# Performance work log

Hardware: AMD Instinct MI355X
Metric: run time of the kernel (lower is better)

Reference implementation:

```python
import jax, jax.numpy as jnp
import numpy as np

B, T, C, H = 4, 2048, 1024, 16
HD = C // H
INIT_SCALE = 0.25

def setup_inputs() -> dict:
    key = jax.random.key(0)
    k1, k2, k3 = jax.random.split(key, 3)
    x = jax.random.normal(k1, (B, T, C), dtype=jnp.float32)
    W_attn = jax.random.normal(k2, (3 * C, C), dtype=jnp.float32) * INIT_SCALE  # torch Linear weight [out,in]
    b_attn = jnp.zeros((3 * C,), dtype=jnp.float32)
    W_proj = jax.random.normal(k3, (C, C), dtype=jnp.float32) * INIT_SCALE
    b_proj = jnp.zeros((C,), dtype=jnp.float32)
    return {"x": x, "W_attn": W_attn, "b_attn": b_attn, "W_proj": W_proj, "b_proj": b_proj}

def reference(x, W_attn, b_attn, W_proj, b_proj):
    # fused QKV projection: [B,T,3C]
    qkv = x @ W_attn.T + b_attn
    q, k, v = jnp.split(qkv, 3, axis=-1)  # each [B,T,C]
    # [B,H,T,HD]
    q = q.reshape(B, T, H, HD).transpose(0, 2, 1, 3)
    k = k.reshape(B, T, H, HD).transpose(0, 2, 1, 3)
    v = v.reshape(B, T, H, HD).transpose(0, 2, 1, 3)
    scale = 1.0 / jnp.sqrt(jnp.asarray(HD, dtype=q.dtype))
    attn = jnp.einsum('bhqd,bhkd->bhqk', q, k) * scale  # [B,H,T,T]
    attn = jax.nn.softmax(attn, axis=-1)
    out = jnp.einsum('bhqk,bhkd->bhqd', attn, v)  # [B,H,T,HD]
    out = out.transpose(0, 2, 1, 3).reshape(B, T, C)
    return out @ W_proj.T + b_proj
```

## Files before the change

kernel.cpp:

```cpp
#include <hip/hip_runtime.h>
#include <hip/hip_bf16.h>

#define BB 4
#define TT 2048
#define CC 1024
#define HH 16
#define HD 64

typedef _Float16 half8 __attribute__((ext_vector_type(8)));
typedef _Float16 half4 __attribute__((ext_vector_type(4)));
typedef _Float16 half2_t __attribute__((ext_vector_type(2)));
typedef float floatx4 __attribute__((ext_vector_type(4)));

__device__ __forceinline__ void async_cp16(const void* g, void* l) {
    __builtin_amdgcn_global_load_lds(
        (const __attribute__((address_space(1))) unsigned int*)g,
        (__attribute__((address_space(3))) unsigned int*)l,
        16, 0, 0);
}

__global__ void cvt_f32_f16(const float* __restrict__ src, _Float16* __restrict__ dst, int n) {
    int i = (blockIdx.x * blockDim.x + threadIdx.x) * 8;
    if (i < n) {
        float4 v0 = *(const float4*)(src + i);
        float4 v1 = *(const float4*)(src + i + 4);
        half8 h;
        h[0] = (_Float16)v0.x; h[1] = (_Float16)v0.y; h[2] = (_Float16)v0.z; h[3] = (_Float16)v0.w;
        h[4] = (_Float16)v1.x; h[5] = (_Float16)v1.y; h[6] = (_Float16)v1.z; h[7] = (_Float16)v1.w;
        *(half8*)(dst + i) = h;
    }
}

template <int EPI>
__global__ __launch_bounds__(256) void hgemm_nt(
    const _Float16* __restrict__ A, const _Float16* __restrict__ Bw,
    const float* __restrict__ bias,
    _Float16* __restrict__ q_out, _Float16* __restrict__ k_out, _Float16* __restrict__ v_out,
    float* __restrict__ c_out,
    int M, int N, int K)
{
    __shared__ __attribute__((aligned(16))) _Float16 As[128 * 32];
    __shared__ __attribute__((aligned(16))) _Float16 Bs[128 * 32];

    const int tid  = threadIdx.x;
    const int lane = tid & 63;
    const int wave = tid >> 6;
    const int quad = lane >> 4;
    const int lc   = lane & 15;
    const int wr   = wave >> 1, wc = wave & 1;
    const size_t bm = (size_t)blockIdx.y * 128;
    const size_t bn = (size_t)blockIdx.x * 128;

    const int r0 = tid >> 2;
    const int ck = (tid & 3) * 8;

    const _Float16* Ap0 = A + (bm + r0) * (size_t)K + ck;
    const _Float16* Ap1 = A + (bm + 64 + r0) * (size_t)K + ck;
    const _Float16* Bp0 = Bw + (bn + r0) * (size_t)K + ck;
    const _Float16* Bp1 = Bw + (bn + 64 + r0) * (size_t)K + ck;
    _Float16* lA0 = As + tid * 8;
    _Float16* lA1 = As + 2048 + tid * 8;
    _Float16* lB0 = Bs + tid * 8;
    _Float16* lB1 = Bs + 2048 + tid * 8;

    floatx4 acc[4][4] = {};

    for (int kk = 0; kk < K; kk += 32) {
        __syncthreads();
        async_cp16(Ap0 + kk, lA0);
        async_cp16(Ap1 + kk, lA1);
        async_cp16(Bp0 + kk, lB0);
        async_cp16(Bp1 + kk, lB1);
        __syncthreads();

        half8 af[4], bf[4];
#pragma unroll
        for (int mt = 0; mt < 4; mt++) af[mt] = *(const half8*)(As + (wr * 64 + mt * 16 + lc) * 32 + quad * 8);
#pragma unroll
        for (int nt = 0; nt < 4; nt++) bf[nt] = *(const half8*)(Bs + (wc * 64 + nt * 16 + lc) * 32 + quad * 8);
#pragma unroll
        for (int mt = 0; mt < 4; mt++)
#pragma unroll
            for (int nt = 0; nt < 4; nt++)
                acc[mt][nt] = __builtin_amdgcn_mfma_f32_16x16x32_f16(af[mt], bf[nt], acc[mt][nt], 0, 0, 0);
    }

#pragma unroll
    for (int mt = 0; mt < 4; mt++) {
        int mbase = (int)bm + wr * 64 + mt * 16 + quad * 4;
#pragma unroll
        for (int nt = 0; nt < 4; nt++) {
            int n = (int)bn + wc * 64 + nt * 16 + lc;
            float bv = bias[n];
#pragma unroll
            for (int r = 0; r < 4; r++) {
                float v = acc[mt][nt][r] + bv;
                int mm = mbase + r;
                if (EPI == 0) {
                    int seg = n >> 10;
                    int cm  = n & 1023;
                    int h = cm >> 6, d = cm & 63;
                    int bb = mm >> 11, t = mm & 2047;
                    size_t dst = (((size_t)(bb * HH + h)) * TT + t) * HD + d;
                    if (seg == 0)      q_out[dst] = (_Float16)(v * 0.18033688f);
                    else if (seg == 1) k_out[dst] = (_Float16)v;
                    else               v_out[dst] = (_Float16)v;
                } else {
                    c_out[(size_t)mm * N + n] = v;
                }
            }
        }
    }
}

__global__ __launch_bounds__(512) void attn_flash(
    const _Float16* __restrict__ Qp, const _Float16* __restrict__ Kp,
    const _Float16* __restrict__ Vp, _Float16* __restrict__ Op)
{
    __shared__ __attribute__((aligned(16))) _Float16 Ks[64][72];
    __shared__ __attribute__((aligned(16))) _Float16 Vt[64][76];

    const int bh   = blockIdx.x;
    const int qt   = blockIdx.y;
    const int tid  = threadIdx.x;
    const int lane = tid & 63;
    const int wave = tid >> 6;
    const int quad = lane >> 4;
    const int lc   = lane & 15;

    const size_t hb = (size_t)bh * TT * HD;
    const _Float16* Kh = Kp + hb;
    const _Float16* Vh = Vp + hb;

    const int q0row = qt * 256 + wave * 32 + lc;
    const int q1row = q0row + 16;
    half8 bq00 = *(const half8*)(Qp + hb + (size_t)q0row * HD + quad * 8);
    half8 bq01 = *(const half8*)(Qp + hb + (size_t)q0row * HD + 32 + quad * 8);
    half8 bq10 = *(const half8*)(Qp + hb + (size_t)q1row * HD + quad * 8);
    half8 bq11 = *(const half8*)(Qp + hb + (size_t)q1row * HD + 32 + quad * 8);

    floatx4 o0[4] = {}, o1[4] = {};
    float m0 = -1e30f, l0 = 0.f, m1 = -1e30f, l1 = 0.f;

    const int sk  = tid >> 3;
    const int sc0 = (tid & 7) * 8;
    const int vkp = tid >> 4;
    const int vd4 = (tid & 15) * 4;

    const _Float16* Kg  = Kh + (size_t)sk * HD + sc0;
    const _Float16* Vg0 = Vh + (size_t)(2 * vkp) * HD + vd4;
    const _Float16* Vg1 = Vg0 + HD;

    for (int kt = 0; kt < TT; kt += 64) {
        const size_t koff = (size_t)kt * HD;
        half8 kv  = *(const half8*)(Kg + koff);
        half4 va0 = *(const half4*)(Vg0 + koff);
        half4 vb0 = *(const half4*)(Vg1 + koff);
        __syncthreads();
        *(half8*)&Ks[sk][sc0] = kv;
#pragma unroll
        for (int j = 0; j < 4; j++) {
            half2_t w; w[0] = va0[j]; w[1] = vb0[j];
            *(half2_t*)&Vt[vd4 + j][2 * vkp] = w;
        }
        __syncthreads();

        floatx4 s0[4], s1[4];
        const floatx4 zf = {0.f, 0.f, 0.f, 0.f};
#pragma unroll
        for (int m = 0; m < 4; m++) {
            half8 a0 = *(const half8*)&Ks[m * 16 + lc][quad * 8];
            half8 a1 = *(const half8*)&Ks[m * 16 + lc][32 + quad * 8];
            s0[m] = __builtin_amdgcn_mfma_f32_16x16x32_f16(a0, bq00, zf, 0, 0, 0);
            s0[m] = __builtin_amdgcn_mfma_f32_16x16x32_f16(a1, bq01, s0[m], 0, 0, 0);
            s1[m] = __builtin_amdgcn_mfma_f32_16x16x32_f16(a0, bq10, zf, 0, 0, 0);
            s1[m] = __builtin_amdgcn_mfma_f32_16x16x32_f16(a1, bq11, s1[m], 0, 0, 0);
        }

        half4 pf0[4], pf1[4];
        {
            float mx = s0[0][0];
#pragma unroll
            for (int m = 0; m < 4; m++)
#pragma unroll
                for (int r = 0; r < 4; r++) mx = fmaxf(mx, s0[m][r]);
            mx = fmaxf(mx, __shfl_xor(mx, 16));
            mx = fmaxf(mx, __shfl_xor(mx, 32));
            float mnew = fmaxf(m0, mx);
            float al = exp2f(m0 - mnew);
            m0 = mnew;
            float rs = 0.f;
#pragma unroll
            for (int m = 0; m < 4; m++) {
                float p0 = exp2f(s0[m][0] - mnew);
                float p1 = exp2f(s0[m][1] - mnew);
                float p2 = exp2f(s0[m][2] - mnew);
                float p3 = exp2f(s0[m][3] - mnew);
                rs += (p0 + p1) + (p2 + p3);
                half4 t;
                t[0] = (_Float16)p0; t[1] = (_Float16)p1;
                t[2] = (_Float16)p2; t[3] = (_Float16)p3;
                pf0[m] = t;
            }
            rs += __shfl_xor(rs, 16);
            rs += __shfl_xor(rs, 32);
            l0 = l0 * al + rs;
#pragma unroll
            for (int dt = 0; dt < 4; dt++) o0[dt] *= al;
        }
        {
            float mx = s1[0][0];
#pragma unroll
            for (int m = 0; m < 4; m++)
#pragma unroll
                for (int r = 0; r < 4; r++) mx = fmaxf(mx, s1[m][r]);
            mx = fmaxf(mx, __shfl_xor(mx, 16));
            mx = fmaxf(mx, __shfl_xor(mx, 32));
            float mnew = fmaxf(m1, mx);
            float al = exp2f(m1 - mnew);
            m1 = mnew;
            float rs = 0.f;
#pragma unroll
            for (int m = 0; m < 4; m++) {
                float p0 = exp2f(s1[m][0] - mnew);
                float p1 = exp2f(s1[m][1] - mnew);
                float p2 = exp2f(s1[m][2] - mnew);
                float p3 = exp2f(s1[m][3] - mnew);
                rs += (p0 + p1) + (p2 + p3);
                half4 t;
                t[0] = (_Float16)p0; t[1] = (_Float16)p1;
                t[2] = (_Float16)p2; t[3] = (_Float16)p3;
                pf1[m] = t;
            }
            rs += __shfl_xor(rs, 16);
            rs += __shfl_xor(rs, 32);
            l1 = l1 * al + rs;
#pragma unroll
            for (int dt = 0; dt < 4; dt++) o1[dt] *= al;
        }

#pragma unroll
        for (int dt = 0; dt < 4; dt++) {
            const _Float16* vr = &Vt[dt * 16 + lc][quad * 4];
#pragma unroll
            for (int m = 0; m < 4; m++) {
                half4 va = *(const half4*)(vr + m * 16);
                o0[dt] = __builtin_amdgcn_mfma_f32_16x16x16f16(va, pf0[m], o0[dt], 0, 0, 0);
                o1[dt] = __builtin_amdgcn_mfma_f32_16x16x16f16(va, pf1[m], o1[dt], 0, 0, 0);
            }
        }
    }

    const int b = bh >> 4, h = bh & 15;
    {
        float inv = 1.0f / l0;
        size_t base = ((size_t)(b * TT + q0row)) * CC + h * HD;
#pragma unroll
        for (int dt = 0; dt < 4; dt++) {
            half4 hv;
#pragma unroll
            for (int r = 0; r < 4; r++) hv[r] = (_Float16)(o0[dt][r] * inv);
            *(half4*)(Op + base + dt * 16 + quad * 4) = hv;
        }
    }
    {
        float inv = 1.0f / l1;
        size_t base = ((size_t)(b * TT + q1row)) * CC + h * HD;
#pragma unroll
        for (int dt = 0; dt < 4; dt++) {
            half4 hv;
#pragma unroll
            for (int r = 0; r < 4; r++) hv[r] = (_Float16)(o1[dt][r] * inv);
            *(half4*)(Op + base + dt * 16 + quad * 4) = hv;
        }
    }
}

extern "C" void kernel_launch(void* const* d_in, const int* in_sizes, int n_in,
                              void* d_out, int out_size, void* d_ws, size_t ws_size,
                              hipStream_t stream) {
    const float* x      = (const float*)d_in[0];
    const float* W_attn = (const float*)d_in[1];
    const float* b_attn = (const float*)d_in[2];
    const float* W_proj = (const float*)d_in[3];
    const float* b_proj = (const float*)d_in[4];
    float* out = (float*)d_out;

    const size_t SZ_XH  = (size_t)BB * TT * CC * 2;
    const size_t SZ_WA  = (size_t)3 * CC * CC * 2;
    const size_t SZ_WP  = (size_t)CC * CC * 2;
    const size_t SZ_QKV = (size_t)BB * HH * TT * HD * 2;
    size_t off = 0;
    _Float16* xh  = (_Float16*)((char*)d_ws + off); off += SZ_XH;
    _Float16* wah = (_Float16*)((char*)d_ws + off); off += SZ_WA;
    _Float16* wph = (_Float16*)((char*)d_ws + off); off += SZ_WP;
    _Float16* Qh  = (_Float16*)((char*)d_ws + off); off += SZ_QKV;
    _Float16* Kh  = (_Float16*)((char*)d_ws + off); off += SZ_QKV;
    _Float16* Vh  = (_Float16*)((char*)d_ws + off); off += SZ_QKV;
    _Float16* Ah  = (_Float16*)((char*)d_ws + off); off += SZ_XH;
    if (ws_size < off) return;

    const int NX  = BB * TT * CC;
    const int NWA = 3 * CC * CC;
    const int NWP = CC * CC;
    cvt_f32_f16<<<NX / 8 / 256, 256, 0, stream>>>(x, xh, NX);
    cvt_f32_f16<<<NWA / 8 / 256, 256, 0, stream>>>(W_attn, wah, NWA);
    cvt_f32_f16<<<NWP / 8 / 256, 256, 0, stream>>>(W_proj, wph, NWP);

    hgemm_nt<0><<<dim3(3 * CC / 128, BB * TT / 128), 256, 0, stream>>>(
        xh, wah, b_attn, Qh, Kh, Vh, nullptr, BB * TT, 3 * CC, CC);

    attn_flash<<<dim3(BB * HH, TT / 256), 512, 0, stream>>>(Qh, Kh, Vh, Ah);

    hgemm_nt<1><<<dim3(CC / 128, BB * TT / 128), 256, 0, stream>>>(
        Ah, wph, b_proj, nullptr, nullptr, nullptr, out, BB * TT, CC, CC);
}
```

Before: 326.5 us.

## Double-buffer GEMM LDS tiles and prefetch next K/V tile in attention

The GEMM kernel now uses two LDS buffers. It issues the async global-to-LDS copy for the next 32-wide K chunk before computing on the current one, so loads overlap the MFMA work instead of stalling between barriers. The attention kernel register-prefetches the next K/V tile right after the LDS store barrier, hiding global latency behind the QK/softmax/PV compute. This costs double the GEMM LDS footprint and extra live registers in attention, which may reduce occupancy. The GEMM relies on the async copy completing by the next __syncthreads, with no explicit vmcnt wait.

```diff
diff --git a/kernel.cpp b/kernel.cpp
--- a/kernel.cpp
+++ b/kernel.cpp
@@ -31,6 +31,28 @@
     }
 }
 
+#define GEMM_CP(base, koffs)                                      \
+    async_cp16(Ap0 + (koffs), (base) + tid * 8);                  \
+    async_cp16(Ap1 + (koffs), (base) + 2048 + tid * 8);           \
+    async_cp16(Bp0 + (koffs), (base) + 4096 + tid * 8);           \
+    async_cp16(Bp1 + (koffs), (base) + 6144 + tid * 8);
+
+#define GEMM_CHUNK(base)                                                        \
+    {                                                                           \
+        half8 af[4], bf[4];                                                     \
+        _Pragma("unroll")                                                       \
+        for (int mt = 0; mt < 4; mt++)                                          \
+            af[mt] = *(const half8*)((base) + (wr * 64 + mt * 16 + lc) * 32 + quad * 8); \
+        _Pragma("unroll")                                                       \
+        for (int nt = 0; nt < 4; nt++)                                          \
+            bf[nt] = *(const half8*)((base) + 4096 + (wc * 64 + nt * 16 + lc) * 32 + quad * 8); \
+        _Pragma("unroll")                                                       \
+        for (int mt = 0; mt < 4; mt++)                                          \
+            _Pragma("unroll")                                                   \
+            for (int nt = 0; nt < 4; nt++)                                      \
+                acc[mt][nt] = __builtin_amdgcn_mfma_f32_16x16x32_f16(af[mt], bf[nt], acc[mt][nt], 0, 0, 0); \
+    }
+
 template <int EPI>
 __global__ __launch_bounds__(256) void hgemm_nt(
     const _Float16* __restrict__ A, const _Float16* __restrict__ Bw,
@@ -39,8 +61,7 @@
     float* __restrict__ c_out,
     int M, int N, int K)
 {
-    __shared__ __attribute__((aligned(16))) _Float16 As[128 * 32];
-    __shared__ __attribute__((aligned(16))) _Float16 Bs[128 * 32];
+    __shared__ __attribute__((aligned(16))) _Float16 Sb[2 * 8192];
 
     const int tid  = threadIdx.x;
     const int lane = tid & 63;
@@ -58,31 +79,17 @@
     const _Float16* Ap1 = A + (bm + 64 + r0) * (size_t)K + ck;
     const _Float16* Bp0 = Bw + (bn + r0) * (size_t)K + ck;
     const _Float16* Bp1 = Bw + (bn + 64 + r0) * (size_t)K + ck;
-    _Float16* lA0 = As + tid * 8;
-    _Float16* lA1 = As + 2048 + tid * 8;
-    _Float16* lB0 = Bs + tid * 8;
-    _Float16* lB1 = Bs + 2048 + tid * 8;
 
     floatx4 acc[4][4] = {};
 
-    for (int kk = 0; kk < K; kk += 32) {
+    GEMM_CP(Sb, 0);
+    for (int kk = 0; kk < K; kk += 64) {
         __syncthreads();
-        async_cp16(Ap0 + kk, lA0);
-        async_cp16(Ap1 + kk, lA1);
-        async_cp16(Bp0 + kk, lB0);
-        async_cp16(Bp1 + kk, lB1);
+        if (kk + 32 < K) { GEMM_CP(Sb + 8192, kk + 32); }
+        GEMM_CHUNK(Sb);
         __syncthreads();
-
-        half8 af[4], bf[4];
-#pragma unroll
-        for (int mt = 0; mt < 4; mt++) af[mt] = *(const half8*)(As + (wr * 64 + mt * 16 + lc) * 32 + quad * 8);
-#pragma unroll
-        for (int nt = 0; nt < 4; nt++) bf[nt] = *(const half8*)(Bs + (wc * 64 + nt * 16 + lc) * 32 + quad * 8);
-#pragma unroll
-        for (int mt = 0; mt < 4; mt++)
-#pragma unroll
-            for (int nt = 0; nt < 4; nt++)
-                acc[mt][nt] = __builtin_amdgcn_mfma_f32_16x16x32_f16(af[mt], bf[nt], acc[mt][nt], 0, 0, 0);
+        if (kk + 64 < K) { GEMM_CP(Sb, kk + 64); }
+        GEMM_CHUNK(Sb + 8192);
     }
 
 #pragma unroll
@@ -151,19 +158,26 @@
     const _Float16* Vg0 = Vh + (size_t)(2 * vkp) * HD + vd4;
     const _Float16* Vg1 = Vg0 + HD;
 
+    half8 kv = *(const half8*)(Kg);
+    half4 va = *(const half4*)(Vg0);
+    half4 vb = *(const half4*)(Vg1);
+
     for (int kt = 0; kt < TT; kt += 64) {
-        const size_t koff = (size_t)kt * HD;
-        half8 kv  = *(const half8*)(Kg + koff);
-        half4 va0 = *(const half4*)(Vg0 + koff);
-        half4 vb0 = *(const half4*)(Vg1 + koff);
         __syncthreads();
         *(half8*)&Ks[sk][sc0] = kv;
 #pragma unroll
         for (int j = 0; j < 4; j++) {
-            half2_t w; w[0] = va0[j]; w[1] = vb0[j];
+            half2_t w; w[0] = va[j]; w[1] = vb[j];
             *(half2_t*)&Vt[vd4 + j][2 * vkp] = w;
         }
         __syncthreads();
+
+        {
+            size_t koff2 = (size_t)((kt + 64) & (TT - 1)) * HD;
+            kv = *(const half8*)(Kg + koff2);
+            va = *(const half4*)(Vg0 + koff2);
+            vb = *(const half4*)(Vg1 + koff2);
+        }
 
         floatx4 s0[4], s1[4];
         const floatx4 zf = {0.f, 0.f, 0.f, 0.f};
@@ -244,9 +258,9 @@
             const _Float16* vr = &Vt[dt * 16 + lc][quad * 4];
 #pragma unroll
             for (int m = 0; m < 4; m++) {
-                half4 va = *(const half4*)(vr + m * 16);
-                o0[dt] = __builtin_amdgcn_mfma_f32_16x16x16f16(va, pf0[m], o0[dt], 0, 0, 0);
-                o1[dt] = __builtin_amdgcn_mfma_f32_16x16x16f16(va, pf1[m], o1[dt], 0, 0, 0);
+                half4 vfr = *(const half4*)(vr + m * 16);
+                o0[dt] = __builtin_amdgcn_mfma_f32_16x16x16f16(vfr, pf0[m], o0[dt], 0, 0, 0);
+                o1[dt] = __builtin_amdgcn_mfma_f32_16x16x16f16(vfr, pf1[m], o1[dt], 0, 0, 0);
             }
         }
     }
```

Result: slower. 354.6 us (+8.6%).
